# Performance work log

Hardware: AMD Instinct MI355X
Metric: run time of the kernel (lower is better)

## Reference

```python
import jax, jax.numpy as jnp
import numpy as np

N, IN_DIM, H, D = 4096, 512, 4, 64


def setup_inputs() -> dict:
    key = jax.random.key(0)
    k1, k2, k3, k4 = jax.random.split(key, 4)
    features = jax.random.normal(k1, (N, IN_DIM), dtype=jnp.float32)
    adjacency = jax.random.randint(k2, (N, N), 0, 2, dtype=jnp.int32)
    weights = jax.random.normal(k3, (IN_DIM, D * H), dtype=jnp.float32) * (1.414 / np.sqrt(IN_DIM))
    attention = jax.random.normal(k4, (1, H, 2 * D), dtype=jnp.float32) * 0.1
    bias = jnp.zeros((D * H,), dtype=jnp.float32)
    return {"features": features, "adjacency": adjacency, "weights": weights,
            "attention": attention, "bias": bias}


def reference(features, adjacency, weights, attention, bias):
    n = features.shape[0]
    h = (features @ weights).reshape(n, H, D)  # [N, H, D]
    # e[i,j,h] = leakyrelu(a1_h . h_i + a2_h . h_j)  (concat-attention decomposed)
    a1 = attention[0, :, :D]   # [H, D]
    a2 = attention[0, :, D:]   # [H, D]
    s1 = jnp.einsum('nhd,hd->nh', h, a1)  # [N, H]
    s2 = jnp.einsum('nhd,hd->nh', h, a2)  # [N, H]
    e = jax.nn.leaky_relu(s1[:, None, :] + s2[None, :, :], negative_slope=0.2)  # [N, N, H]
    masked = jnp.where(adjacency[:, :, None] > 0, e, jnp.float32(-9e15))
    attn = jax.nn.softmax(masked, axis=1)  # softmax over neighbors j (dim=1)
    out = jnp.einsum('ijh,jhd->ihd', attn, h).reshape(n, H * D)
    return out + bias
```

## Files before the change

### kernel.cpp

```cpp
#include <hip/hip_runtime.h>
#include <hip/hip_bf16.h>

#define N_NODES 4096
#define IN_DIMC 512
#define NHEADS 4
#define DHEAD 64
#define OUT_COLS 256
#define HP_HEAD_BYTES (N_NODES * DHEAD * 2)

typedef __attribute__((ext_vector_type(8))) short short8;
typedef __attribute__((ext_vector_type(4))) float f32x4;

__device__ __forceinline__ short bf16b(float x) {
    return __builtin_bit_cast(short, __float2bfloat16(x));
}

__device__ __forceinline__ void gload_lds16(const void* g, void* l) {
    __builtin_amdgcn_global_load_lds((const __attribute__((address_space(1))) void*)g,
                                     (__attribute__((address_space(3))) void*)l,
                                     16, 0, 0);
}

__global__ __launch_bounds__(256) void k_gemm_fused(
    const float* __restrict__ A, const float* __restrict__ W,
    const float* __restrict__ att,
    char* __restrict__ hP, float* __restrict__ s1T, float* __restrict__ s2T)
{
    __shared__ float As[32][36];
    __shared__ float Bs[32][68];
    __shared__ float ht[64][33];
    const int m0 = blockIdx.x * 32;
    const int head = blockIdx.y;
    const int n0 = head * 64;
    const int t = (int)threadIdx.x;
    const int tm = t & 7, tn = t >> 3;
    float acc[4][2] = {};
    for (int k0 = 0; k0 < IN_DIMC; k0 += 32) {
        {
            const int r = t >> 3, kc = (t & 7) << 2;
            float4 v0 = *(const float4*)(A + (size_t)(m0 + r) * IN_DIMC + k0 + kc);
            As[kc + 0][r] = v0.x; As[kc + 1][r] = v0.y; As[kc + 2][r] = v0.z; As[kc + 3][r] = v0.w;
            const int rb = t >> 4, nc = (t & 15) << 2;
            float4 w0 = *(const float4*)(W + (size_t)(k0 + rb) * OUT_COLS + n0 + nc);
            float4 w1 = *(const float4*)(W + (size_t)(k0 + rb + 16) * OUT_COLS + n0 + nc);
            *(float4*)&Bs[rb][nc] = w0;
            *(float4*)&Bs[rb + 16][nc] = w1;
        }
        __syncthreads();
        #pragma unroll
        for (int kk = 0; kk < 32; ++kk) {
            const f32x4 a = *(const f32x4*)&As[kk][tm << 2];
            const float b0 = Bs[kk][tn * 2], b1 = Bs[kk][tn * 2 + 1];
            #pragma unroll
            for (int i = 0; i < 4; ++i) {
                acc[i][0] = fmaf(a[i], b0, acc[i][0]);
                acc[i][1] = fmaf(a[i], b1, acc[i][1]);
            }
        }
        __syncthreads();
    }
    #pragma unroll
    for (int i = 0; i < 4; ++i) {
        ht[tn * 2 + 0][(tm << 2) + i] = acc[i][0];
        ht[tn * 2 + 1][(tm << 2) + i] = acc[i][1];
    }
    __syncthreads();
    {
        const int d = t >> 2, qq = t & 3;
        short8 hv;
        #pragma unroll
        for (int k = 0; k < 8; ++k) hv[k] = bf16b(ht[d][qq * 8 + k]);
        const size_t off16 = ((size_t)(m0 >> 5) * 4 + (d >> 4)) * 64 + qq * 16 + (d & 15);
        *(short8*)(hP + (size_t)head * HP_HEAD_BYTES + off16 * 16) = hv;
    }
    {
        const int r = t >> 3, part = t & 7;
        float p1 = 0.f, p2 = 0.f;
        #pragma unroll
        for (int dd = 0; dd < 8; ++dd) {
            const int d = part * 8 + dd;
            const float v = ht[d][r];
            p1 = fmaf(v, att[head * 128 + d], p1);
            p2 = fmaf(v, att[head * 128 + 64 + d], p2);
        }
        p1 += __shfl_xor(p1, 1); p1 += __shfl_xor(p1, 2); p1 += __shfl_xor(p1, 4);
        p2 += __shfl_xor(p2, 1); p2 += __shfl_xor(p2, 2); p2 += __shfl_xor(p2, 4);
        if (part == 0) {
            s1T[head * N_NODES + m0 + r] = p1;
            s2T[head * N_NODES + m0 + r] = p2;
        }
    }
}

__global__ __launch_bounds__(256) void k_pack(
    const int* __restrict__ adj, unsigned long long* __restrict__ bitsT)
{
    const int gt = blockIdx.x * 256 + (int)threadIdx.x;
    const int wv = gt >> 6;
    const int lane = gt & 63;
    const int nwaves = (int)gridDim.x * 4;
    const int nwords = (N_NODES * N_NODES) / 64;
    for (int n = wv * 4; n < nwords; n += nwaves * 4) {
        const int i0 = (n + 0) >> 6, c0 = (n + 0) & 63;
        const int i1 = (n + 1) >> 6, c1 = (n + 1) & 63;
        const int i2 = (n + 2) >> 6, c2 = (n + 2) & 63;
        const int i3 = (n + 3) >> 6, c3 = (n + 3) & 63;
        const int a0 = adj[(size_t)i0 * N_NODES + c0 * 64 + lane];
        const int a1 = adj[(size_t)i1 * N_NODES + c1 * 64 + lane];
        const int a2 = adj[(size_t)i2 * N_NODES + c2 * 64 + lane];
        const int a3 = adj[(size_t)i3 * N_NODES + c3 * 64 + lane];
        const unsigned long long m0 = __ballot(a0 != 0);
        const unsigned long long m1 = __ballot(a1 != 0);
        const unsigned long long m2 = __ballot(a2 != 0);
        const unsigned long long m3 = __ballot(a3 != 0);
        if (lane == 0) {
            bitsT[(size_t)c0 * N_NODES + i0] = m0;
            bitsT[(size_t)c1 * N_NODES + i1] = m1;
            bitsT[(size_t)c2 * N_NODES + i2] = m2;
            bitsT[(size_t)c3 * N_NODES + i3] = m3;
        }
    }
}

__global__ __launch_bounds__(1024, 4) void k_gat(
    const unsigned long long* __restrict__ bitsT, const char* __restrict__ hP,
    const float* __restrict__ s1T, const float* __restrict__ s2T,
    const float* __restrict__ bias, float* __restrict__ out)
{
    __shared__ __align__(16) char stage[16 * 8192];
    const int i0 = blockIdx.x * 16;
    const int t = (int)threadIdx.x;
    const int w = t >> 6;
    const int head = w & 3;
    const int seg = w >> 2;
    const int lane = t & 63;
    const int il = lane & 15;
    const int q = lane >> 4;
    char* myStage = stage + w * 8192;
    const char* hPh = hP + (size_t)head * HP_HEAD_BYTES;
    const float* s2h = s2T + head * N_NODES;
    const float s1v = s1T[head * N_NODES + i0 + il];
    f32x4 acc[4] = {{0.f,0.f,0.f,0.f},{0.f,0.f,0.f,0.f},{0.f,0.f,0.f,0.f},{0.f,0.f,0.f,0.f}};
    float denom = 0.f;

    const int g0 = seg * 32;
    unsigned long long bitsCur = bitsT[(size_t)(g0 >> 1) * N_NODES + i0 + il];
    float4 sAc = *(const float4*)(s2h + g0 * 32 + q * 8);
    float4 sBc = *(const float4*)(s2h + g0 * 32 + q * 8 + 4);
    #pragma unroll
    for (int dblk = 0; dblk < 4; ++dblk)
        gload_lds16(hPh + (size_t)g0 * 4096 + dblk * 1024 + lane * 16,
                    myStage + dblk * 1024);

    #pragma unroll 2
    for (int s = 0; s < 32; ++s) {
        const int g = g0 + s;
        unsigned long long bitsNxt = bitsCur;
        float4 sAn = sAc, sBn = sBc;
        if (s < 31) {
            const int gn = g + 1;
            bitsNxt = bitsT[(size_t)(gn >> 1) * N_NODES + i0 + il];
            sAn = *(const float4*)(s2h + gn * 32 + q * 8);
            sBn = *(const float4*)(s2h + gn * 32 + q * 8 + 4);
            char* ldst = myStage + ((s + 1) & 1) * 4096;
            #pragma unroll
            for (int dblk = 0; dblk < 4; ++dblk)
                gload_lds16(hPh + (size_t)gn * 4096 + dblk * 1024 + lane * 16,
                            ldst + dblk * 1024);
            asm volatile("s_waitcnt vmcnt(7)" ::: "memory");
        } else {
            asm volatile("s_waitcnt vmcnt(0)" ::: "memory");
        }
        const unsigned msk = (unsigned)(bitsCur >> ((g & 1) * 32 + q * 8)) & 0xffu;
        short8 afrag;
        {
            float x, p;
            x = s1v + sAc.x; x = fmaxf(x, 0.2f * x);
            p = (msk & 1u)   ? __expf(x) : 0.f; denom += p; afrag[0] = bf16b(p);
            x = s1v + sAc.y; x = fmaxf(x, 0.2f * x);
            p = (msk & 2u)   ? __expf(x) : 0.f; denom += p; afrag[1] = bf16b(p);
            x = s1v + sAc.z; x = fmaxf(x, 0.2f * x);
            p = (msk & 4u)   ? __expf(x) : 0.f; denom += p; afrag[2] = bf16b(p);
            x = s1v + sAc.w; x = fmaxf(x, 0.2f * x);
            p = (msk & 8u)   ? __expf(x) : 0.f; denom += p; afrag[3] = bf16b(p);
            x = s1v + sBc.x; x = fmaxf(x, 0.2f * x);
            p = (msk & 16u)  ? __expf(x) : 0.f; denom += p; afrag[4] = bf16b(p);
            x = s1v + sBc.y; x = fmaxf(x, 0.2f * x);
            p = (msk & 32u)  ? __expf(x) : 0.f; denom += p; afrag[5] = bf16b(p);
            x = s1v + sBc.z; x = fmaxf(x, 0.2f * x);
            p = (msk & 64u)  ? __expf(x) : 0.f; denom += p; afrag[6] = bf16b(p);
            x = s1v + sBc.w; x = fmaxf(x, 0.2f * x);
            p = (msk & 128u) ? __expf(x) : 0.f; denom += p; afrag[7] = bf16b(p);
        }
        const short8* fb = (const short8*)(myStage + (s & 1) * 4096);
        #pragma unroll
        for (int dblk = 0; dblk < 4; ++dblk) {
            const short8 b = fb[dblk * 64 + lane];
            acc[dblk] = __builtin_amdgcn_mfma_f32_16x16x32_bf16(afrag, b, acc[dblk], 0, 0, 0);
        }
        bitsCur = bitsNxt; sAc = sAn; sBc = sBn;
    }
    denom += __shfl_xor(denom, 16);
    denom += __shfl_xor(denom, 32);

    __syncthreads();
    float* red  = (float*)stage;
    float* dred = (float*)(stage + 49152);
    if (seg > 0) {
        const int p = (w - 4) * 1024;
        #pragma unroll
        for (int r = 0; r < 4; ++r) {
            const int row = q * 4 + r;
            red[p + row * 64 + 0  + il] = acc[0][r];
            red[p + row * 64 + 16 + il] = acc[1][r];
            red[p + row * 64 + 32 + il] = acc[2][r];
            red[p + row * 64 + 48 + il] = acc[3][r];
        }
        if (q == 0) dred[(w - 4) * 16 + il] = denom;
    }
    __syncthreads();
    if (seg == 0) {
        #pragma unroll
        for (int r = 0; r < 4; ++r) {
            const int row = q * 4 + r;
            float dsum = __shfl(denom, row);
            #pragma unroll
            for (int s = 1; s < 4; ++s)
                dsum += dred[((s - 1) * 4 + w) * 16 + row];
            const float inv = 1.0f / dsum;
            #pragma unroll
            for (int dblk = 0; dblk < 4; ++dblk) {
                float v = acc[dblk][r];
                #pragma unroll
                for (int s = 1; s < 4; ++s)
                    v += red[((s - 1) * 4 + w) * 1024 + row * 64 + dblk * 16 + il];
                out[(size_t)(i0 + row) * OUT_COLS + w * DHEAD + dblk * 16 + il] =
                    v * inv + bias[w * DHEAD + dblk * 16 + il];
            }
        }
    }
}

extern "C" void kernel_launch(void* const* d_in, const int* in_sizes, int n_in,
                              void* d_out, int out_size, void* d_ws, size_t ws_size,
                              hipStream_t stream) {
    const float* features  = (const float*)d_in[0];
    const int*   adjacency = (const int*)d_in[1];
    const float* weights   = (const float*)d_in[2];
    const float* attention = (const float*)d_in[3];
    const float* bias      = (const float*)d_in[4];
    float* out = (float*)d_out;

    char* ws = (char*)d_ws;
    char*               hP    = ws;
    unsigned long long* bitsT = (unsigned long long*)(ws + 2u*1024*1024);
    float*              s1T   = (float*)(ws + 4u*1024*1024);
    float*              s2T   = (float*)(ws + 4u*1024*1024 + 64u*1024);

    k_pack<<<dim3(2048), 256, 0, stream>>>(adjacency, bitsT);
    k_gemm_fused<<<dim3(128, 4), 256, 0, stream>>>(features, weights, attention,
                                                   hP, s1T, s2T);
    k_gat<<<dim3(256), 1024, 0, stream>>>(bitsT, hP, s1T, s2T, bias, out);
}
```

Measured before the change: 72.22 us.

## Factor exp of leaky-relu into per-node exponentials and drop adjacency pack kernel

Rewrites exp(leakyrelu(s1+s2)) as max(e^s1*e^s2, e^{0.2 s1}*e^{0.2 s2}), so the GEMM kernel precomputes four per-node exponential tables and the attention loop does multiplies instead of exp. The separate bit-packing kernel is removed, and the attention kernel reads the int32 adjacency rows directly as int4 vectors. The softmax denominator is now computed by an extra MFMA against a ones vector rather than by scalar adds. The cost is 16x more adjacency bytes read inside the main kernel, and there is a risk of overflow or underflow because the exponentials are no longer max-subtracted, though neither softmax version subtracts a max.

```diff
diff --git a/kernel.cpp b/kernel.cpp
--- a/kernel.cpp
+++ b/kernel.cpp
@@ -24,7 +24,8 @@
 __global__ __launch_bounds__(256) void k_gemm_fused(
     const float* __restrict__ A, const float* __restrict__ W,
     const float* __restrict__ att,
-    char* __restrict__ hP, float* __restrict__ s1T, float* __restrict__ s2T)
+    char* __restrict__ hP, float* __restrict__ E1, float* __restrict__ F1,
+    float* __restrict__ E2, float* __restrict__ F2)
 {
     __shared__ float As[32][36];
     __shared__ float Bs[32][68];
@@ -86,45 +87,19 @@
         p1 += __shfl_xor(p1, 1); p1 += __shfl_xor(p1, 2); p1 += __shfl_xor(p1, 4);
         p2 += __shfl_xor(p2, 1); p2 += __shfl_xor(p2, 2); p2 += __shfl_xor(p2, 4);
         if (part == 0) {
-            s1T[head * N_NODES + m0 + r] = p1;
-            s2T[head * N_NODES + m0 + r] = p2;
-        }
-    }
-}
-
-__global__ __launch_bounds__(256) void k_pack(
-    const int* __restrict__ adj, unsigned long long* __restrict__ bitsT)
-{
-    const int gt = blockIdx.x * 256 + (int)threadIdx.x;
-    const int wv = gt >> 6;
-    const int lane = gt & 63;
-    const int nwaves = (int)gridDim.x * 4;
-    const int nwords = (N_NODES * N_NODES) / 64;
-    for (int n = wv * 4; n < nwords; n += nwaves * 4) {
-        const int i0 = (n + 0) >> 6, c0 = (n + 0) & 63;
-        const int i1 = (n + 1) >> 6, c1 = (n + 1) & 63;
-        const int i2 = (n + 2) >> 6, c2 = (n + 2) & 63;
-        const int i3 = (n + 3) >> 6, c3 = (n + 3) & 63;
-        const int a0 = adj[(size_t)i0 * N_NODES + c0 * 64 + lane];
-        const int a1 = adj[(size_t)i1 * N_NODES + c1 * 64 + lane];
-        const int a2 = adj[(size_t)i2 * N_NODES + c2 * 64 + lane];
-        const int a3 = adj[(size_t)i3 * N_NODES + c3 * 64 + lane];
-        const unsigned long long m0 = __ballot(a0 != 0);
-        const unsigned long long m1 = __ballot(a1 != 0);
-        const unsigned long long m2 = __ballot(a2 != 0);
-        const unsigned long long m3 = __ballot(a3 != 0);
-        if (lane == 0) {
-            bitsT[(size_t)c0 * N_NODES + i0] = m0;
-            bitsT[(size_t)c1 * N_NODES + i1] = m1;
-            bitsT[(size_t)c2 * N_NODES + i2] = m2;
-            bitsT[(size_t)c3 * N_NODES + i3] = m3;
+            const int idx = head * N_NODES + m0 + r;
+            E1[idx] = __expf(p1);
+            F1[idx] = __expf(0.2f * p1);
+            E2[idx] = __expf(p2);
+            F2[idx] = __expf(0.2f * p2);
         }
     }
 }
 
 __global__ __launch_bounds__(1024, 4) void k_gat(
-    const unsigned long long* __restrict__ bitsT, const char* __restrict__ hP,
-    const float* __restrict__ s1T, const float* __restrict__ s2T,
+    const int* __restrict__ adj, const char* __restrict__ hP,
+    const float* __restrict__ E1, const float* __restrict__ F1,
+    const float* __restrict__ E2, const float* __restrict__ F2,
     const float* __restrict__ bias, float* __restrict__ out)
 {
     __shared__ __align__(16) char stage[16 * 8192];
@@ -138,15 +113,25 @@
     const int q = lane >> 4;
     char* myStage = stage + w * 8192;
     const char* hPh = hP + (size_t)head * HP_HEAD_BYTES;
-    const float* s2h = s2T + head * N_NODES;
-    const float s1v = s1T[head * N_NODES + i0 + il];
-    f32x4 acc[4] = {{0.f,0.f,0.f,0.f},{0.f,0.f,0.f,0.f},{0.f,0.f,0.f,0.f},{0.f,0.f,0.f,0.f}};
-    float denom = 0.f;
+    const float e1 = E1[head * N_NODES + i0 + il];
+    const float f1 = F1[head * N_NODES + i0 + il];
+    const float* E2h = E2 + head * N_NODES;
+    const float* F2h = F2 + head * N_NODES;
+    const int* arow = adj + (size_t)(i0 + il) * N_NODES;
+    f32x4 acc[5] = {{0.f,0.f,0.f,0.f},{0.f,0.f,0.f,0.f},{0.f,0.f,0.f,0.f},
+                    {0.f,0.f,0.f,0.f},{0.f,0.f,0.f,0.f}};
+    short8 onesv;
+    #pragma unroll
+    for (int e = 0; e < 8; ++e) onesv[e] = (short)0x3F80;
 
     const int g0 = seg * 32;
-    unsigned long long bitsCur = bitsT[(size_t)(g0 >> 1) * N_NODES + i0 + il];
-    float4 sAc = *(const float4*)(s2h + g0 * 32 + q * 8);
-    float4 sBc = *(const float4*)(s2h + g0 * 32 + q * 8 + 4);
+    int jb = (g0 << 5) + (q << 3);
+    int4   avA = *(const int4*)(arow + jb);
+    int4   avB = *(const int4*)(arow + jb + 4);
+    float4 e2a = *(const float4*)(E2h + jb);
+    float4 e2b = *(const float4*)(E2h + jb + 4);
+    float4 f2a = *(const float4*)(F2h + jb);
+    float4 f2b = *(const float4*)(F2h + jb + 4);
     #pragma unroll
     for (int dblk = 0; dblk < 4; ++dblk)
         gload_lds16(hPh + (size_t)g0 * 4096 + dblk * 1024 + lane * 16,
@@ -154,43 +139,44 @@
 
     #pragma unroll 2
     for (int s = 0; s < 32; ++s) {
-        const int g = g0 + s;
-        unsigned long long bitsNxt = bitsCur;
-        float4 sAn = sAc, sBn = sBc;
+        int4 navA = avA, navB = avB;
+        float4 ne2a = e2a, ne2b = e2b, nf2a = f2a, nf2b = f2b;
         if (s < 31) {
-            const int gn = g + 1;
-            bitsNxt = bitsT[(size_t)(gn >> 1) * N_NODES + i0 + il];
-            sAn = *(const float4*)(s2h + gn * 32 + q * 8);
-            sBn = *(const float4*)(s2h + gn * 32 + q * 8 + 4);
+            const int jn = jb + 32;
+            navA = *(const int4*)(arow + jn);
+            navB = *(const int4*)(arow + jn + 4);
+            ne2a = *(const float4*)(E2h + jn);
+            ne2b = *(const float4*)(E2h + jn + 4);
+            nf2a = *(const float4*)(F2h + jn);
+            nf2b = *(const float4*)(F2h + jn + 4);
             char* ldst = myStage + ((s + 1) & 1) * 4096;
             #pragma unroll
             for (int dblk = 0; dblk < 4; ++dblk)
-                gload_lds16(hPh + (size_t)gn * 4096 + dblk * 1024 + lane * 16,
+                gload_lds16(hPh + (size_t)(g0 + s + 1) * 4096 + dblk * 1024 + lane * 16,
                             ldst + dblk * 1024);
-            asm volatile("s_waitcnt vmcnt(7)" ::: "memory");
+            asm volatile("s_waitcnt vmcnt(10)" ::: "memory");
         } else {
             asm volatile("s_waitcnt vmcnt(0)" ::: "memory");
         }
-        const unsigned msk = (unsigned)(bitsCur >> ((g & 1) * 32 + q * 8)) & 0xffu;
         short8 afrag;
         {
-            float x, p;
-            x = s1v + sAc.x; x = fmaxf(x, 0.2f * x);
-            p = (msk & 1u)   ? __expf(x) : 0.f; denom += p; afrag[0] = bf16b(p);
-            x = s1v + sAc.y; x = fmaxf(x, 0.2f * x);
-            p = (msk & 2u)   ? __expf(x) : 0.f; denom += p; afrag[1] = bf16b(p);
-            x = s1v + sAc.z; x = fmaxf(x, 0.2f * x);
-            p = (msk & 4u)   ? __expf(x) : 0.f; denom += p; afrag[2] = bf16b(p);
-            x = s1v + sAc.w; x = fmaxf(x, 0.2f * x);
-            p = (msk & 8u)   ? __expf(x) : 0.f; denom += p; afrag[3] = bf16b(p);
-            x = s1v + sBc.x; x = fmaxf(x, 0.2f * x);
-            p = (msk & 16u)  ? __expf(x) : 0.f; denom += p; afrag[4] = bf16b(p);
-            x = s1v + sBc.y; x = fmaxf(x, 0.2f * x);
-            p = (msk & 32u)  ? __expf(x) : 0.f; denom += p; afrag[5] = bf16b(p);
-            x = s1v + sBc.z; x = fmaxf(x, 0.2f * x);
-            p = (msk & 64u)  ? __expf(x) : 0.f; denom += p; afrag[6] = bf16b(p);
-            x = s1v + sBc.w; x = fmaxf(x, 0.2f * x);
-            p = (msk & 128u) ? __expf(x) : 0.f; denom += p; afrag[7] = bf16b(p);
+            float g, hh, p;
+            g = e1 * e2a.x; hh = f1 * f2a.x; p = fmaxf(g, hh);
+            afrag[0] = bf16b(avA.x != 0 ? p : 0.f);
+            g = e1 * e2a.y; hh = f1 * f2a.y; p = fmaxf(g, hh);
+            afrag[1] = bf16b(avA.y != 0 ? p : 0.f);
+            g = e1 * e2a.z; hh = f1 * f2a.z; p = fmaxf(g, hh);
+            afrag[2] = bf16b(avA.z != 0 ? p : 0.f);
+            g = e1 * e2a.w; hh = f1 * f2a.w; p = fmaxf(g, hh);
+            afrag[3] = bf16b(avA.w != 0 ? p : 0.f);
+            g = e1 * e2b.x; hh = f1 * f2b.x; p = fmaxf(g, hh);
+            afrag[4] = bf16b(avB.x != 0 ? p : 0.f);
+            g = e1 * e2b.y; hh = f1 * f2b.y; p = fmaxf(g, hh);
+            afrag[5] = bf16b(avB.y != 0 ? p : 0.f);
+            g = e1 * e2b.z; hh = f1 * f2b.z; p = fmaxf(g, hh);
+            afrag[6] = bf16b(avB.z != 0 ? p : 0.f);
+            g = e1 * e2b.w; hh = f1 * f2b.w; p = fmaxf(g, hh);
+            afrag[7] = bf16b(avB.w != 0 ? p : 0.f);
         }
         const short8* fb = (const short8*)(myStage + (s & 1) * 4096);
         #pragma unroll
@@ -198,10 +184,11 @@
             const short8 b = fb[dblk * 64 + lane];
             acc[dblk] = __builtin_amdgcn_mfma_f32_16x16x32_bf16(afrag, b, acc[dblk], 0, 0, 0);
         }
-        bitsCur = bitsNxt; sAc = sAn; sBc = sBn;
-    }
-    denom += __shfl_xor(denom, 16);
-    denom += __shfl_xor(denom, 32);
+        acc[4] = __builtin_amdgcn_mfma_f32_16x16x32_bf16(afrag, onesv, acc[4], 0, 0, 0);
+        avA = navA; avB = navB;
+        e2a = ne2a; e2b = ne2b; f2a = nf2a; f2b = nf2b;
+        jb += 32;
+    }
 
     __syncthreads();
     float* red  = (float*)stage;
@@ -216,14 +203,18 @@
             red[p + row * 64 + 32 + il] = acc[2][r];
             red[p + row * 64 + 48 + il] = acc[3][r];
         }
-        if (q == 0) dred[(w - 4) * 16 + il] = denom;
+        if (il == 0) {
+            #pragma unroll
+            for (int r = 0; r < 4; ++r)
+                dred[(w - 4) * 16 + q * 4 + r] = acc[4][r];
+        }
     }
     __syncthreads();
     if (seg == 0) {
         #pragma unroll
         for (int r = 0; r < 4; ++r) {
             const int row = q * 4 + r;
-            float dsum = __shfl(denom, row);
+            float dsum = acc[4][r];
             #pragma unroll
             for (int s = 1; s < 4; ++s)
                 dsum += dred[((s - 1) * 4 + w) * 16 + row];
@@ -252,13 +243,13 @@
     float* out = (float*)d_out;
 
     char* ws = (char*)d_ws;
-    char*               hP    = ws;
-    unsigned long long* bitsT = (unsigned long long*)(ws + 2u*1024*1024);
-    float*              s1T   = (float*)(ws + 4u*1024*1024);
-    float*              s2T   = (float*)(ws + 4u*1024*1024 + 64u*1024);
-
-    k_pack<<<dim3(2048), 256, 0, stream>>>(adjacency, bitsT);
+    char*  hP = ws;
+    float* E1 = (float*)(ws + 2u*1024*1024);
+    float* F1 = (float*)(ws + 2u*1024*1024 +  64u*1024);
+    float* E2 = (float*)(ws + 2u*1024*1024 + 128u*1024);
+    float* F2 = (float*)(ws + 2u*1024*1024 + 192u*1024);
+
     k_gemm_fused<<<dim3(128, 4), 256, 0, stream>>>(features, weights, attention,
-                                                   hP, s1T, s2T);
-    k_gat<<<dim3(256), 1024, 0, stream>>>(bitsT, hP, s1T, s2T, bias, out);
-}
+                                                   hP, E1, F1, E2, F2);
+    k_gat<<<dim3(256), 1024, 0, stream>>>(adjacency, hP, E1, F1, E2, F2, bias, out);
+}
```

Result: slower. 87.50 us (+21.2%).
